# Kernel optimization log

Measured on AMD Instinct MI355X. Metric: run time of the kernel, lower is better.

Reference implementation:

```python
import jax, jax.numpy as jnp
import numpy as np


def setup_inputs() -> dict:
    key = jax.random.key(0)
    ks = jax.random.split(key, 6)
    B, S, D, H = 8, 1024, 1024, 16
    dk = D // H
    inputs = jax.random.normal(ks[0], (B, S, D), dtype=jnp.float32)
    mask = jnp.ones((B, S), dtype=jnp.float32)
    scale = 0.02
    W_q = jax.random.normal(ks[1], (H, D, dk), dtype=jnp.float32) * scale
    W_k = jax.random.normal(ks[2], (H, D, dk), dtype=jnp.float32) * scale
    W_v = jax.random.normal(ks[3], (D, D), dtype=jnp.float32) * scale
    W_o = jax.random.normal(ks[4], (D, D), dtype=jnp.float32) * scale
    return {"inputs": inputs, "mask": mask, "W_q": W_q, "W_k": W_k,
            "W_v": W_v, "W_o": W_o}


def reference(inputs, mask, W_q, W_k, W_v, W_o):
    B, S, D = inputs.shape
    H, _, dk = W_q.shape
    # combined causal + padding mask: 1.0 where attention is disallowed
    causal = 1.0 - jnp.tril(jnp.ones((S, S), dtype=jnp.float32))  # [S,S]
    input_mask = mask[:, None, :] * mask[:, :, None]              # [B,S,S]
    bad = jnp.maximum(causal[None, :, :], 1.0 - input_mask)       # [B,S,S]

    V = jnp.einsum('bsd,de->bse', inputs, W_v)                    # shared values
    Q = jnp.einsum('bsd,hdk->bhsk', inputs, W_q)
    K = jnp.einsum('bsd,hdk->bhsk', inputs, W_k)
    scores = jnp.einsum('bhqk,bhsk->bhqs', Q, K) / jnp.sqrt(jnp.float32(dk))
    scores = scores - bad[:, None, :, :] * 1e9
    attn = jax.nn.softmax(scores, axis=-1)                        # [B,H,S,S]
    attn_avg = jnp.mean(attn, axis=1)                             # [B,S,S]
    Hout = jnp.einsum('bqs,bse->bqe', attn_avg, V)
    output = jnp.einsum('bqe,ed->bqd', Hout, W_o)
    return (output, attn_avg)
```

## Files before the change

### kernel.cpp

```cpp
#include <hip/hip_runtime.h>

typedef unsigned short ushort;
typedef __bf16 bf16x8 __attribute__((ext_vector_type(8)));
typedef float f32x4 __attribute__((ext_vector_type(4)));
typedef unsigned short us8v __attribute__((ext_vector_type(8)));

__device__ __forceinline__ ushort f2bf(float f) {
  unsigned u = __builtin_bit_cast(unsigned, f);
  u += 0x7FFFu + ((u >> 16) & 1u);
  return (ushort)(u >> 16);
}

__device__ __forceinline__ bf16x8 ld_bf16x8(const ushort* p) {
  uint4 v = *(const uint4*)p;
  return __builtin_bit_cast(bf16x8, v);
}

__device__ __forceinline__ void gl16(const ushort* g, ushort* l) {
  __builtin_amdgcn_global_load_lds(
      (const __attribute__((address_space(1))) void*)g,
      (__attribute__((address_space(3))) void*)l, 16, 0, 0);
}

__global__ __launch_bounds__(256) void pack_x(const float* __restrict__ in,
                                              ushort* __restrict__ out) {
  long i = (long)blockIdx.x * 256 + threadIdx.x;
  const float4* s = (const float4*)in;
  float4 a = s[i * 2], b = s[i * 2 + 1];
  us8v o;
  o[0] = f2bf(a.x); o[1] = f2bf(a.y); o[2] = f2bf(a.z); o[3] = f2bf(a.w);
  o[4] = f2bf(b.x); o[5] = f2bf(b.y); o[6] = f2bf(b.z); o[7] = f2bf(b.w);
  *(us8v*)&out[i * 8] = o;
}

__global__ __launch_bounds__(256) void transpose_pack(
    const float* __restrict__ src, ushort* __restrict__ dst,
    int sC, int dLd, long sBatch, long dBatch, float scale) {
  src += (long)blockIdx.z * sBatch;
  dst += (long)blockIdx.z * dBatch;
  const int r0 = blockIdx.y * 64, c0 = blockIdx.x * 64;
  __shared__ ushort T[64 * 68];
  const int t = threadIdx.x;
#pragma unroll
  for (int i = 0; i < 4; ++i) {
    int ch = t + 256 * i;
    int r = ch >> 4, c4 = ch & 15;
    float4 v = *(const float4*)&src[(long)(r0 + r) * sC + c0 + c4 * 4];
    T[(c4 * 4 + 0) * 68 + r] = f2bf(v.x * scale);
    T[(c4 * 4 + 1) * 68 + r] = f2bf(v.y * scale);
    T[(c4 * 4 + 2) * 68 + r] = f2bf(v.z * scale);
    T[(c4 * 4 + 3) * 68 + r] = f2bf(v.w * scale);
  }
  __syncthreads();
#pragma unroll
  for (int i = 0; i < 4; ++i) {
    int ch = t + 256 * i;
    int c = ch >> 4, r4 = ch & 15;
    ushort4 o;
    o.x = T[c * 68 + r4 * 4 + 0];
    o.y = T[c * 68 + r4 * 4 + 1];
    o.z = T[c * 68 + r4 * 4 + 2];
    o.w = T[c * 68 + r4 * 4 + 3];
    *(ushort4*)&dst[(long)(c0 + c) * dLd + r0 + r4 * 4] = o;
  }
}

template <int EPI, bool CAUSAL, int SWZ>
__global__ __launch_bounds__(256, 3) void gemm4(
    const ushort* __restrict__ A, const ushort* __restrict__ Bt,
    int N, int K, long aB, long bB,
    ushort* __restrict__ O_q, ushort* __restrict__ O_k, ushort* __restrict__ O_v,
    ushort* __restrict__ O_b, long oB,
    float* __restrict__ O_f) {
  __shared__ __align__(16) ushort As[128 * 64];
  __shared__ __align__(16) ushort Bs[128 * 64];
  const int tid = threadIdx.x;
  const int lane = tid & 63, w = tid >> 6;
  const int lr = lane & 15, lg = lane >> 4;

  const int nx = gridDim.x, ny = gridDim.y;
  long nwg = (long)nx * ny * gridDim.z;
  long hwid = blockIdx.x + (long)nx * (blockIdx.y + (long)ny * blockIdx.z);
  long cpx = nwg >> 3;
  long sid = (hwid & 7) * cpx + (hwid >> 3);
  int bx, by, z;
  if (SWZ == 1) {
    by = (int)(sid % ny);
    int t2 = (int)(sid / ny);
    bx = t2 % nx;
    z = t2 / nx;
  } else {
    bx = (int)(sid % nx);
    int t2 = (int)(sid / nx);
    by = t2 % ny;
    z = t2 / ny;
  }

  const int row0 = by * 128, col0 = bx * 128;
  A += (long)z * aB;
  Bt += (long)z * bB;
  const int wr = (w >> 1) * 64, wc = (w & 1) * 64;

  f32x4 acc[4][4] = {};
  const int kmax = CAUSAL ? (K < row0 + 128 ? K : row0 + 128) : K;
  const int nk = kmax >> 6;

  for (int kt = 0; kt < nk; ++kt) {
    const int k0 = kt << 6;
    __syncthreads();
#pragma unroll
    for (int j = 0; j < 4; ++j) {
      int c = tid + 256 * j;
      int r = c >> 3, c8 = (c & 7) ^ (r & 7);
      gl16(&A[(long)(row0 + r) * K + k0 + c8 * 8], &As[c * 8]);
      gl16(&Bt[(long)(col0 + r) * K + k0 + c8 * 8], &Bs[c * 8]);
    }
    __syncthreads();
#pragma unroll
    for (int kk = 0; kk < 2; ++kk) {
      bf16x8 af[4], bfr[4];
#pragma unroll
      for (int m = 0; m < 4; ++m) {
        int row = wr + m * 16 + lr;
        int c8 = (kk * 4 + lg) ^ (row & 7);
        af[m] = ld_bf16x8(&As[row * 64 + c8 * 8]);
      }
#pragma unroll
      for (int n = 0; n < 4; ++n) {
        int row = wc + n * 16 + lr;
        int c8 = (kk * 4 + lg) ^ (row & 7);
        bfr[n] = ld_bf16x8(&Bs[row * 64 + c8 * 8]);
      }
#pragma unroll
      for (int m = 0; m < 4; ++m)
#pragma unroll
        for (int n = 0; n < 4; ++n)
          acc[m][n] = __builtin_amdgcn_mfma_f32_16x16x32_bf16(af[m], bfr[n], acc[m][n], 0, 0, 0);
    }
  }

#pragma unroll
  for (int m = 0; m < 4; ++m)
#pragma unroll
    for (int n = 0; n < 4; ++n)
#pragma unroll
      for (int r = 0; r < 4; ++r) {
        int gr = row0 + wr + m * 16 + lg * 4 + r;
        int gc = col0 + wc + n * 16 + lr;
        float v = acc[m][n][r];
        if (EPI == 0) {
          int b = gr >> 10, s = gr & 1023;
          if (gc < 1024) {
            int h = gc >> 6, kq = gc & 63;
            O_q[(((long)(b * 16 + h) << 10) + s) * 64 + kq] = f2bf(v);
          } else if (gc < 2048) {
            int n2 = gc - 1024;
            int h = n2 >> 6, kq = n2 & 63;
            O_k[(((long)(b * 16 + h) << 10) + s) * 64 + kq] = f2bf(v);
          } else {
            int e = gc - 2048;
            O_v[((long)(b << 10) + e) * 1024 + s] = f2bf(v);
          }
        } else if (EPI == 1) {
          (O_b + (long)z * oB)[(long)gr * N + gc] = f2bf(v);
        } else {
          O_f[(long)gr * N + gc] = v;
        }
      }
}

__global__ __launch_bounds__(512, 2) void attn16(
    const ushort* __restrict__ Qb, const ushort* __restrict__ Kb,
    const float* __restrict__ mask, float* __restrict__ attn_out,
    ushort* __restrict__ attnb) {
  __shared__ __align__(16) ushort Ks[2][4 * 128 * 64];
  __shared__ float redS[2][8][16];
  const int tid = threadIdx.x;
  const int lane = tid & 63, w = tid >> 6;
  const int lr = lane & 15, lg = lane >> 4;
  const int hw = blockIdx.x + 32 * blockIdx.y;
  const int b = hw & 7;
  const int x2 = hw >> 3;
  const int q0a = x2 * 16;
  const int q0b = (63 - x2) * 16;
  const int NTb = ((63 - x2) >> 3) + 1;
  const int n1 = (NTb - 4) << 10;
  const int NTWa = (x2 >> 3) + 1;
  const int NTWb = ((63 - x2) >> 3) + 1;

  float mqa[4], mqb[4], ms[8];
#pragma unroll
  for (int r = 0; r < 4; ++r) {
    mqa[r] = mask[b * 1024 + q0a + lg * 4 + r];
    mqb[r] = mask[b * 1024 + q0b + lg * 4 + r];
  }
#pragma unroll
  for (int t = 0; t < 8; ++t) ms[t] = mask[b * 1024 + t * 128 + w * 16 + lr];

  auto stageG = [&](int buf, int t0, int nch, int h) {
    const long hb = ((long)(b * 16 + h)) << 10;
#pragma unroll 2
    for (int i = tid; i < nch; i += 512) {
      int j = i >> 10, r = (i >> 3) & 127, c8 = i & 7;
      gl16(&Kb[(hb + (t0 + j) * 128 + r) * 64 + ((c8 ^ (r & 7)) << 3)],
           &Ks[buf][i * 8]);
    }
  };

  const int row = w * 16 + lr;
  const int cs0 = ((0 + lg) ^ (row & 7)) * 8;
  const int cs1 = ((4 + lg) ^ (row & 7)) * 8;

  stageG(0, 0, 4096, 0);
  __syncthreads();

  f32x4 acca[4] = {};
  f32x4 accb[8] = {};
#pragma unroll 1
  for (int h = 0; h < 16; ++h) {
    const long hb = ((long)(b * 16 + h)) << 10;
    const bf16x8 qa0 = ld_bf16x8(&Qb[(hb + q0a + lr) * 64 + lg * 8]);
    const bf16x8 qa1 = ld_bf16x8(&Qb[(hb + q0a + lr) * 64 + 32 + lg * 8]);
    const bf16x8 qb0 = ld_bf16x8(&Qb[(hb + q0b + lr) * 64 + lg * 8]);
    const bf16x8 qb1 = ld_bf16x8(&Qb[(hb + q0b + lr) * 64 + 32 + lg * 8]);

    stageG(1, 4, n1, h);

    f32x4 sca[4], scb[8];
    float psa[4] = {0.f, 0.f, 0.f, 0.f}, psb[4] = {0.f, 0.f, 0.f, 0.f};
#pragma unroll
    for (int t = 0; t < 4; ++t) {
      const int sb = t * 128 + w * 16;
      const ushort* kr = &Ks[0][(t * 128 + row) * 64];
      bf16x8 k0 = ld_bf16x8(kr + cs0);
      bf16x8 k1 = ld_bf16x8(kr + cs1);
      {
        f32x4 d = {};
        d = __builtin_amdgcn_mfma_f32_16x16x32_bf16(qb0, k0, d, 0, 0, 0);
        d = __builtin_amdgcn_mfma_f32_16x16x32_bf16(qb1, k1, d, 0, 0, 0);
#pragma unroll
        for (int r = 0; r < 4; ++r) {
          float e = __expf(d[r]) * (mqb[r] * ms[t]);
          scb[t][r] = e;
          psb[r] += e;
        }
      }
      if (sb <= q0a) {
        f32x4 d = {};
        d = __builtin_amdgcn_mfma_f32_16x16x32_bf16(qa0, k0, d, 0, 0, 0);
        d = __builtin_amdgcn_mfma_f32_16x16x32_bf16(qa1, k1, d, 0, 0, 0);
#pragma unroll
        for (int r = 0; r < 4; ++r) {
          float e = __expf(d[r]) * (mqa[r] * ms[t]);
          if (sb == q0a) e = (lr <= lg * 4 + r) ? e : 0.f;
          sca[t][r] = e;
          psa[r] += e;
        }
      }
    }
    __syncthreads();

    if (h < 15) stageG(0, 0, 4096, h + 1);

#pragma unroll
    for (int t = 4; t < 8; ++t) {
      const int sb = t * 128 + w * 16;
      if (sb <= q0b) {
        const ushort* kr = &Ks[1][((t - 4) * 128 + row) * 64];
        bf16x8 k0 = ld_bf16x8(kr + cs0);
        bf16x8 k1 = ld_bf16x8(kr + cs1);
        f32x4 d = {};
        d = __builtin_amdgcn_mfma_f32_16x16x32_bf16(qb0, k0, d, 0, 0, 0);
        d = __builtin_amdgcn_mfma_f32_16x16x32_bf16(qb1, k1, d, 0, 0, 0);
#pragma unroll
        for (int r = 0; r < 4; ++r) {
          float e = __expf(d[r]) * (mqb[r] * ms[t]);
          if (sb == q0b) e = (lr <= lg * 4 + r) ? e : 0.f;
          scb[t][r] = e;
          psb[r] += e;
        }
      }
    }
#pragma unroll
    for (int r = 0; r < 4; ++r) {
      psa[r] += __shfl_xor(psa[r], 1);
      psa[r] += __shfl_xor(psa[r], 2);
      psa[r] += __shfl_xor(psa[r], 4);
      psa[r] += __shfl_xor(psa[r], 8);
      psb[r] += __shfl_xor(psb[r], 1);
      psb[r] += __shfl_xor(psb[r], 2);
      psb[r] += __shfl_xor(psb[r], 4);
      psb[r] += __shfl_xor(psb[r], 8);
    }
    if (lr == 0) {
#pragma unroll
      for (int r = 0; r < 4; ++r) {
        redS[0][w][lg * 4 + r] = psa[r];
        redS[1][w][lg * 4 + r] = psb[r];
      }
    }
    __syncthreads();

#pragma unroll
    for (int r = 0; r < 4; ++r) {
      float ta = 0.f, tb = 0.f;
#pragma unroll
      for (int ww = 0; ww < 8; ++ww) {
        ta += redS[0][ww][lg * 4 + r];
        tb += redS[1][ww][lg * 4 + r];
      }
      float ra = __builtin_amdgcn_rcpf(ta);
      float rb = __builtin_amdgcn_rcpf(tb);
#pragma unroll
      for (int t = 0; t < 4; ++t) {
        const int sb = t * 128 + w * 16;
        if (sb <= q0a) acca[t][r] += sca[t][r] * ra;
      }
#pragma unroll
      for (int t = 0; t < 8; ++t) {
        const int sb = t * 128 + w * 16;
        if (sb <= q0b) accb[t][r] += scb[t][r] * rb;
      }
    }
  }

#pragma unroll
  for (int t = 0; t < 8; ++t) {
    int s = t * 128 + w * 16 + lr;
#pragma unroll
    for (int r = 0; r < 4; ++r) {
      {
        int q = q0a + lg * 4 + r;
        float v = (t < 4 ? acca[t][r] : 0.f) * 0.0625f;
        long o = ((long)(b * 1024 + q) << 10) + s;
        attn_out[o] = v;
        if (t < NTWa) attnb[o] = f2bf(v);
      }
      {
        int q = q0b + lg * 4 + r;
        float v = accb[t][r] * 0.0625f;
        long o = ((long)(b * 1024 + q) << 10) + s;
        attn_out[o] = v;
        if (t < NTWb) attnb[o] = f2bf(v);
      }
    }
  }
}

extern "C" void kernel_launch(void* const* d_in, const int* in_sizes, int n_in,
                              void* d_out, int out_size, void* d_ws, size_t ws_size,
                              hipStream_t stream) {
  const float* inputs = (const float*)d_in[0];
  const float* mask   = (const float*)d_in[1];
  const float* W_q    = (const float*)d_in[2];
  const float* W_k    = (const float*)d_in[3];
  const float* W_v    = (const float*)d_in[4];
  const float* W_o    = (const float*)d_in[5];
  float* out = (float*)d_out;

  ushort* Xb    = (ushort*)d_ws;
  ushort* WqkvT = Xb + 8192L * 1024;
  ushort* WoT   = WqkvT + 3072L * 1024;
  ushort* Qb    = WoT + 1024L * 1024;
  ushort* Kb    = Qb + 8L * 16 * 1024 * 64;
  ushort* Vt    = Kb + 8L * 16 * 1024 * 64;
  ushort* attnb = Vt + 8L * 1024 * 1024;
  ushort* Houtb = attnb + 8L * 1024 * 1024;

  pack_x<<<4096, 256, 0, stream>>>(inputs, Xb);
  transpose_pack<<<dim3(1, 16, 16), 256, 0, stream>>>(W_q, WqkvT, 64, 1024,
                                                      65536L, 64L * 1024, 0.125f);
  transpose_pack<<<dim3(1, 16, 16), 256, 0, stream>>>(W_k, WqkvT + 1024L * 1024, 64, 1024,
                                                      65536L, 64L * 1024, 1.0f);
  transpose_pack<<<dim3(16, 16, 1), 256, 0, stream>>>(W_v, WqkvT + 2048L * 1024, 1024, 1024,
                                                      0L, 0L, 1.0f);
  transpose_pack<<<dim3(16, 16, 1), 256, 0, stream>>>(W_o, WoT, 1024, 1024,
                                                      0L, 0L, 1.0f);
  gemm4<0, false, 1><<<dim3(24, 64, 1), 256, 0, stream>>>(
      Xb, WqkvT, 3072, 1024, 0L, 0L, Qb, Kb, Vt, nullptr, 0L, nullptr);
  attn16<<<dim3(32, 8), 512, 0, stream>>>(Qb, Kb, mask, out + 8388608L, attnb);
  gemm4<1, true, 0><<<dim3(8, 8, 8), 256, 0, stream>>>(
      attnb, Vt, 1024, 1024, 1048576L, 1048576L,
      nullptr, nullptr, nullptr, Houtb, 1048576L, nullptr);
  gemm4<2, false, 1><<<dim3(8, 64, 1), 256, 0, stream>>>(
      Houtb, WoT, 1024, 1024, 0L, 0L,
      nullptr, nullptr, nullptr, nullptr, 0L, out);
}
```

Before: 248.0 us.

## Double-buffer GEMM LDS with prefetch and enlarge tiles to 256x128 with 512 threads

```diff
diff --git a/kernel.cpp b/kernel.cpp
--- a/kernel.cpp
+++ b/kernel.cpp
@@ -66,56 +66,59 @@
 }
 
 template <int EPI, bool CAUSAL, int SWZ>
-__global__ __launch_bounds__(256, 3) void gemm4(
+__global__ __launch_bounds__(512, 1) void gemm2ph(
     const ushort* __restrict__ A, const ushort* __restrict__ Bt,
     int N, int K, long aB, long bB,
     ushort* __restrict__ O_q, ushort* __restrict__ O_k, ushort* __restrict__ O_v,
     ushort* __restrict__ O_b, long oB,
     float* __restrict__ O_f) {
-  __shared__ __align__(16) ushort As[128 * 64];
-  __shared__ __align__(16) ushort Bs[128 * 64];
+  __shared__ __align__(16) ushort As[2][256 * 64];
+  __shared__ __align__(16) ushort Bs[2][128 * 64];
   const int tid = threadIdx.x;
   const int lane = tid & 63, w = tid >> 6;
   const int lr = lane & 15, lg = lane >> 4;
 
   const int nx = gridDim.x, ny = gridDim.y;
-  long nwg = (long)nx * ny * gridDim.z;
-  long hwid = blockIdx.x + (long)nx * (blockIdx.y + (long)ny * blockIdx.z);
-  long cpx = nwg >> 3;
-  long sid = (hwid & 7) * cpx + (hwid >> 3);
+  long hw = blockIdx.x + (long)nx * (blockIdx.y + (long)ny * blockIdx.z);
+  int k8 = (int)(hw & 7);
+  long l = hw >> 3;
   int bx, by, z;
   if (SWZ == 1) {
-    by = (int)(sid % ny);
-    int t2 = (int)(sid / ny);
-    bx = t2 % nx;
-    z = t2 / nx;
+    const int BH = ny >> 3;
+    by = k8 * BH + (int)(l % BH);
+    bx = (int)(l / BH);
+    z = 0;
   } else {
-    bx = (int)(sid % nx);
-    int t2 = (int)(sid / nx);
-    by = t2 % ny;
-    z = t2 / ny;
-  }
-
-  const int row0 = by * 128, col0 = bx * 128;
+    z = k8;
+    by = (int)(l % ny);
+    bx = (int)(l / ny);
+  }
+
+  const int row0 = by * 256, col0 = bx * 128;
   A += (long)z * aB;
   Bt += (long)z * bB;
   const int wr = (w >> 1) * 64, wc = (w & 1) * 64;
 
   f32x4 acc[4][4] = {};
-  const int kmax = CAUSAL ? (K < row0 + 128 ? K : row0 + 128) : K;
+  const int kmax = CAUSAL ? (K < row0 + 256 ? K : row0 + 256) : K;
   const int nk = kmax >> 6;
 
-  for (int kt = 0; kt < nk; ++kt) {
+  auto stage = [&](int buf, int kt) {
     const int k0 = kt << 6;
-    __syncthreads();
 #pragma unroll
     for (int j = 0; j < 4; ++j) {
-      int c = tid + 256 * j;
+      int c = tid + 512 * j;
       int r = c >> 3, c8 = (c & 7) ^ (r & 7);
-      gl16(&A[(long)(row0 + r) * K + k0 + c8 * 8], &As[c * 8]);
-      gl16(&Bt[(long)(col0 + r) * K + k0 + c8 * 8], &Bs[c * 8]);
-    }
-    __syncthreads();
+      gl16(&A[(long)(row0 + r) * K + k0 + c8 * 8], &As[buf][c * 8]);
+    }
+#pragma unroll
+    for (int j = 0; j < 2; ++j) {
+      int c = tid + 512 * j;
+      int r = c >> 3, c8 = (c & 7) ^ (r & 7);
+      gl16(&Bt[(long)(col0 + r) * K + k0 + c8 * 8], &Bs[buf][c * 8]);
+    }
+  };
+  auto compute = [&](int buf) {
 #pragma unroll
     for (int kk = 0; kk < 2; ++kk) {
       bf16x8 af[4], bfr[4];
@@ -123,21 +126,38 @@
       for (int m = 0; m < 4; ++m) {
         int row = wr + m * 16 + lr;
         int c8 = (kk * 4 + lg) ^ (row & 7);
-        af[m] = ld_bf16x8(&As[row * 64 + c8 * 8]);
+        af[m] = ld_bf16x8(&As[buf][row * 64 + c8 * 8]);
       }
 #pragma unroll
       for (int n = 0; n < 4; ++n) {
         int row = wc + n * 16 + lr;
         int c8 = (kk * 4 + lg) ^ (row & 7);
-        bfr[n] = ld_bf16x8(&Bs[row * 64 + c8 * 8]);
-      }
+        bfr[n] = ld_bf16x8(&Bs[buf][row * 64 + c8 * 8]);
+      }
+      __builtin_amdgcn_s_setprio(1);
 #pragma unroll
       for (int m = 0; m < 4; ++m)
 #pragma unroll
         for (int n = 0; n < 4; ++n)
           acc[m][n] = __builtin_amdgcn_mfma_f32_16x16x32_bf16(af[m], bfr[n], acc[m][n], 0, 0, 0);
-    }
-  }
+      __builtin_amdgcn_s_setprio(0);
+    }
+  };
+
+  stage(0, 0);
+  asm volatile("s_waitcnt vmcnt(0)" ::: "memory");
+  __builtin_amdgcn_s_barrier();
+  __builtin_amdgcn_sched_barrier(0);
+  int buf = 0;
+  for (int kt = 0; kt < nk - 1; ++kt) {
+    stage(buf ^ 1, kt + 1);
+    compute(buf);
+    asm volatile("s_waitcnt vmcnt(0)" ::: "memory");
+    __builtin_amdgcn_s_barrier();
+    __builtin_amdgcn_sched_barrier(0);
+    buf ^= 1;
+  }
+  compute(buf);
 
 #pragma unroll
   for (int m = 0; m < 4; ++m)
@@ -185,8 +205,8 @@
   const int q0b = (63 - x2) * 16;
   const int NTb = ((63 - x2) >> 3) + 1;
   const int n1 = (NTb - 4) << 10;
-  const int NTWa = (x2 >> 3) + 1;
-  const int NTWb = ((63 - x2) >> 3) + 1;
+  const int NTWa = (x2 >> 4) * 2 + 2;
+  const int NTWb = ((63 - x2) >> 4) * 2 + 2;
 
   float mqa[4], mqb[4], ms[8];
 #pragma unroll
@@ -376,13 +396,13 @@
                                                       0L, 0L, 1.0f);
   transpose_pack<<<dim3(16, 16, 1), 256, 0, stream>>>(W_o, WoT, 1024, 1024,
                                                       0L, 0L, 1.0f);
-  gemm4<0, false, 1><<<dim3(24, 64, 1), 256, 0, stream>>>(
+  gemm2ph<0, false, 1><<<dim3(24, 32, 1), 512, 0, stream>>>(
       Xb, WqkvT, 3072, 1024, 0L, 0L, Qb, Kb, Vt, nullptr, 0L, nullptr);
   attn16<<<dim3(32, 8), 512, 0, stream>>>(Qb, Kb, mask, out + 8388608L, attnb);
-  gemm4<1, true, 0><<<dim3(8, 8, 8), 256, 0, stream>>>(
+  gemm2ph<1, true, 0><<<dim3(8, 4, 8), 512, 0, stream>>>(
       attnb, Vt, 1024, 1024, 1048576L, 1048576L,
       nullptr, nullptr, nullptr, Houtb, 1048576L, nullptr);
-  gemm4<2, false, 1><<<dim3(8, 64, 1), 256, 0, stream>>>(
+  gemm2ph<2, false, 1><<<dim3(8, 32, 1), 512, 0, stream>>>(
       Houtb, WoT, 1024, 1024, 0L, 0L,
       nullptr, nullptr, nullptr, nullptr, 0L, out);
 }
```

New measurement: 234.4 us. 5.5% less time.
